# Optimization experiments

Measured on AMD Instinct MI355X. Metric: run time of the kernel, lower is better.

## Reference

```python
import jax, jax.numpy as jnp
import numpy as np

D_MODEL = 1024
EXPAND = 2
D_INNER = EXPAND * D_MODEL   # 2048
D_STATE = 16
D_CONV = 4
DT_RANK = 64                  # ceil(d_model / 16)
BATCH = 2
SEQLEN = 1024
DT_MIN, DT_MAX = 0.001, 0.1


def setup_inputs() -> dict:
    key = jax.random.key(0)
    ks = jax.random.split(key, 10)
    s = 0.02
    # dt bias init per Mamba: inv-softplus of dt sampled log-uniform in [dt_min, dt_max]
    u = jax.random.uniform(ks[0], (D_INNER,), jnp.float32)
    dt = jnp.exp(u * (np.log(DT_MAX) - np.log(DT_MIN)) + np.log(DT_MIN))
    dt = jnp.clip(dt, 1e-4, None)
    inv_dt = dt + jnp.log(-jnp.expm1(-dt))
    dt_std = DT_RANK ** -0.5
    A_log = jnp.log(jnp.tile(jnp.arange(1, D_STATE + 1, dtype=jnp.float32), (D_INNER, 1)))
    return {
        "hidden_states": jax.random.normal(ks[1], (BATCH, SEQLEN, D_MODEL), jnp.float32),
        "in_proj_w": jax.random.normal(ks[2], (2 * D_INNER, D_MODEL), jnp.float32) * s,
        "conv1d_w": jax.random.normal(ks[3], (D_INNER, D_CONV), jnp.float32) * s,
        "conv1d_b": jnp.zeros((D_INNER,), jnp.float32),
        "x_proj_w": jax.random.normal(ks[4], (DT_RANK + 2 * D_STATE, D_INNER), jnp.float32) * s,
        "dt_proj_w": jax.random.uniform(ks[5], (D_INNER, DT_RANK), jnp.float32, -dt_std, dt_std),
        "dt_proj_b": inv_dt,
        "A_log": A_log,
        "D_skip": jnp.ones((D_INNER,), jnp.float32),
        "out_proj_w": jax.random.normal(ks[6], (D_MODEL, D_INNER), jnp.float32) * s,
    }


def _mamba_forward(hidden_states, in_proj_w, conv1d_w, conv1d_b, x_proj_w,
                   dt_proj_w, dt_proj_b, A_log, D_skip, out_proj_w):
    B_, L, _ = hidden_states.shape
    # in_proj: (b, l, d_model) -> (b, l, 2*d_inner); split into x and gate z
    xz = jnp.einsum('bld,ed->ble', hidden_states, in_proj_w)
    x, z = xz[..., :D_INNER], xz[..., D_INNER:]
    # causal depthwise conv1d over time (pad left K-1, truncate to L) + SiLU
    xp = jnp.pad(x, ((0, 0), (D_CONV - 1, 0), (0, 0)))
    xc = conv1d_b
    acc = jnp.zeros_like(x)
    for k in range(D_CONV):  # tiny fixed kernel loop
        acc = acc + conv1d_w[:, k] * xp[:, k:k + L, :]
    xc = jax.nn.silu(acc + conv1d_b)
    # input-dependent dt / B / C
    x_dbl = jnp.einsum('bld,rd->blr', xc, x_proj_w)
    dt_lr = x_dbl[..., :DT_RANK]
    Bm = x_dbl[..., DT_RANK:DT_RANK + D_STATE]        # (b, l, n)
    Cm = x_dbl[..., DT_RANK + D_STATE:]               # (b, l, n)
    delta = jax.nn.softplus(jnp.einsum('blr,dr->bld', dt_lr, dt_proj_w) + dt_proj_b)
    A = -jnp.exp(A_log)                               # (d, n)

    def step(state, inputs):
        delta_t, B_t, C_t, u_t = inputs               # (b,d) (b,n) (b,n) (b,d)
        dA = jnp.exp(delta_t[..., None] * A)          # (b, d, n)
        state = state * dA + (delta_t * u_t)[..., None] * B_t[:, None, :]
        y_t = jnp.einsum('bdn,bn->bd', state, C_t)
        return state, y_t

    init = jnp.zeros((B_, D_INNER, D_STATE), delta.dtype)
    scan_in = (jnp.swapaxes(delta, 0, 1), jnp.swapaxes(Bm, 0, 1),
               jnp.swapaxes(Cm, 0, 1), jnp.swapaxes(xc, 0, 1))
    _, ys = jax.lax.scan(step, init, scan_in)         # ys: (l, b, d)
    y = jnp.swapaxes(ys, 0, 1)
    y = y + xc * D_skip                               # skip connection
    y = y * jax.nn.silu(z)                            # gate
    return jnp.einsum('bld,md->blm', y, out_proj_w)   # out_proj (no bias)


def reference(hidden_states, in_proj_w, conv1d_w, conv1d_b, x_proj_w,
              dt_proj_w, dt_proj_b, A_log, D_skip, out_proj_w):
    return _mamba_forward(hidden_states, in_proj_w, conv1d_w, conv1d_b, x_proj_w,
                          dt_proj_w, dt_proj_b, A_log, D_skip, out_proj_w)
```

## Files before the change

### kernel.cpp

```cpp
#include <hip/hip_runtime.h>
#include <hip/hip_bf16.h>
#include <math.h>
#include <stdint.h>

#define D_MODEL 1024
#define D_INNER 2048
#define D_STATE 16
#define D_CONV  4
#define DT_RANK 64
#define BATCH   2
#define SEQLEN  1024
#define M_TOK   (BATCH * SEQLEN)
#define XDBL_W  (DT_RANK + 2 * D_STATE)
#define CHUNKS  16
#define CLEN    (SEQLEN / CHUNKS)
#define KSPLIT  8

typedef unsigned short us16;
typedef __bf16 bf16x8 __attribute__((ext_vector_type(8)));
typedef float floatx4 __attribute__((ext_vector_type(4)));

__device__ __forceinline__ float silu_f(float v) {
    return v / (1.0f + __expf(-v));
}
__device__ __forceinline__ float softplus_f(float v) {
    return v > 20.0f ? v : log1pf(__expf(v));
}
__device__ __forceinline__ us16 f2bf(float f) {
    unsigned u = __float_as_uint(f);
    u += 0x7FFF + ((u >> 16) & 1);
    return (us16)(u >> 16);
}
__device__ __forceinline__ float bf2f(us16 h) {
    return __uint_as_float(((unsigned)h) << 16);
}

__device__ __forceinline__ void gload_lds16(const us16* g, us16* l) {
    auto* l3 = reinterpret_cast<__attribute__((address_space(3))) us16*>(
        reinterpret_cast<uintptr_t>(l));
    auto* g1 = reinterpret_cast<const __attribute__((address_space(1))) us16*>(
        reinterpret_cast<uintptr_t>(g));
    __builtin_amdgcn_global_load_lds(g1, l3, 16, 0, 0);
}

__global__ __launch_bounds__(256)
void split_bf16(const float* __restrict__ src, us16* __restrict__ hi,
                us16* __restrict__ lo) {
    const int i = (blockIdx.x * 256 + threadIdx.x) * 4;
    const float4 v = *(const float4*)(src + i);
    us16 h0 = f2bf(v.x), h1 = f2bf(v.y), h2 = f2bf(v.z), h3 = f2bf(v.w);
    ushort4 hv = {h0, h1, h2, h3};
    ushort4 lv = {f2bf(v.x - bf2f(h0)), f2bf(v.y - bf2f(h1)),
                  f2bf(v.z - bf2f(h2)), f2bf(v.w - bf2f(h3))};
    *(ushort4*)(hi + i) = hv;
    *(ushort4*)(lo + i) = lv;
}

template<int BN, int MODE>
__global__ __launch_bounds__(256)
void gemm_mfma3(const us16* __restrict__ Ah, const us16* __restrict__ Al,
                const us16* __restrict__ Wh, const us16* __restrict__ Wl,
                int lda, int kLen, float* __restrict__ C0,
                float* __restrict__ C1, int ldc)
{
    constexpr int BM = 128;
    constexpr int NT = BN / 32;
    __shared__ us16 sAh[BM * 32];
    __shared__ us16 sAl[BM * 32];
    __shared__ us16 sWh[BN * 32];
    __shared__ us16 sWl[BN * 32];

    const int tid  = threadIdx.x;
    const int wave = tid >> 6;
    const int lane = tid & 63;
    const int wm   = wave & 1;
    const int wn   = wave >> 1;
    const int m0   = blockIdx.y * BM;
    const int n0   = blockIdx.x * BN;
    const int kBeg = blockIdx.z * kLen;
    const int quad = lane >> 4;
    const int l15  = lane & 15;
    const int sr   = lane >> 2;
    const int spos = lane & 3;

    floatx4 acc[4][NT] = {};

    for (int k0 = 0; k0 < kLen; k0 += 32) {
        __syncthreads();
        {
            int s = wave;
            int row = s * 16 + sr;
            int c = spos ^ ((row >> 1) & 3);
            size_t go = (size_t)(m0 + row) * lda + kBeg + k0 + c * 8;
            gload_lds16(Ah + go, sAh + s * 512);
            gload_lds16(Al + go, sAl + s * 512);
            s = wave + 4;
            row = s * 16 + sr;
            c = spos ^ ((row >> 1) & 3);
            go = (size_t)(m0 + row) * lda + kBeg + k0 + c * 8;
            gload_lds16(Ah + go, sAh + s * 512);
            gload_lds16(Al + go, sAl + s * 512);
        }
        {
            int s = wave;
            int row = s * 16 + sr;
            int c = spos ^ ((row >> 1) & 3);
            size_t go = (size_t)(n0 + row) * lda + kBeg + k0 + c * 8;
            gload_lds16(Wh + go, sWh + s * 512);
            gload_lds16(Wl + go, sWl + s * 512);
            if (BN == 128) {
                s = wave + 4;
                row = s * 16 + sr;
                c = spos ^ ((row >> 1) & 3);
                go = (size_t)(n0 + row) * lda + kBeg + k0 + c * 8;
                gload_lds16(Wh + go, sWh + s * 512);
                gload_lds16(Wl + go, sWl + s * 512);
            }
        }
        __syncthreads();

        bf16x8 ah[4], al[4], bh[NT], bl[NT];
#pragma unroll
        for (int i = 0; i < 4; i++) {
            const int r = wm * 64 + i * 16 + l15;
            const int off = r * 32 + ((quad ^ ((r >> 1) & 3)) * 8);
            ah[i] = *(const bf16x8*)(sAh + off);
            al[i] = *(const bf16x8*)(sAl + off);
        }
#pragma unroll
        for (int j = 0; j < NT; j++) {
            const int r = wn * (BN / 2) + j * 16 + l15;
            const int off = r * 32 + ((quad ^ ((r >> 1) & 3)) * 8);
            bh[j] = *(const bf16x8*)(sWh + off);
            bl[j] = *(const bf16x8*)(sWl + off);
        }
#pragma unroll
        for (int i = 0; i < 4; i++)
#pragma unroll
            for (int j = 0; j < NT; j++) {
                acc[i][j] = __builtin_amdgcn_mfma_f32_16x16x32_bf16(
                    ah[i], bh[j], acc[i][j], 0, 0, 0);
                acc[i][j] = __builtin_amdgcn_mfma_f32_16x16x32_bf16(
                    al[i], bh[j], acc[i][j], 0, 0, 0);
                acc[i][j] = __builtin_amdgcn_mfma_f32_16x16x32_bf16(
                    ah[i], bl[j], acc[i][j], 0, 0, 0);
            }
    }

#pragma unroll
    for (int i = 0; i < 4; i++) {
        const int rowb = m0 + wm * 64 + i * 16 + quad * 4;
#pragma unroll
        for (int j = 0; j < NT; j++) {
            const int col = n0 + wn * (BN / 2) + j * 16 + l15;
#pragma unroll
            for (int r = 0; r < 4; r++) {
                const float v = acc[i][j][r];
                const size_t rr = (size_t)(rowb + r);
                if (MODE == 1) {
                    if (n0 < D_INNER) C0[rr * D_INNER + col] = v;
                    else              C1[rr * D_INNER + (col - D_INNER)] = v;
                } else {
                    C0[((size_t)blockIdx.z * M_TOK + rr) * ldc + col] = v;
                }
            }
        }
    }
}

__global__ __launch_bounds__(256)
void add2_kernel(const float* __restrict__ part, float* __restrict__ out)
{
    const int i = (blockIdx.x * 256 + threadIdx.x) * 4;
    float4 a = *(const float4*)(part + i);
    const float4 b = *(const float4*)(part + (size_t)M_TOK * D_MODEL + i);
    a.x += b.x; a.y += b.y; a.z += b.z; a.w += b.w;
    *(float4*)(out + i) = a;
}

template<int MODE>
__global__ __launch_bounds__(256)
void gemm_nt(const float* __restrict__ A, int lda,
             const float* __restrict__ W, int ldw,
             float* __restrict__ C0, float* __restrict__ C1, int ldc,
             const float* __restrict__ bias,
             int M, int N, int K)
{
    __shared__ float As[16][68];
    __shared__ float Ws[16][68];

    const int tid  = threadIdx.x;
    const int tx   = tid & 15;
    const int ty   = tid >> 4;
    const int n0   = blockIdx.x * 64;
    const int m0   = blockIdx.y * 64;
    const int lrow = tid >> 2;
    const int lkq  = tid & 3;

    float acc[4][4] = {};

    for (int k0 = 0; k0 < K; k0 += 16) {
        const float4 av = *(const float4*)(A + (size_t)(m0 + lrow) * lda + k0 + lkq * 4);
        const int wn = n0 + lrow;
        float4 wv = make_float4(0.f, 0.f, 0.f, 0.f);
        if (wn < N)
            wv = *(const float4*)(W + (size_t)wn * ldw + k0 + lkq * 4);

        __syncthreads();
        As[lkq * 4 + 0][lrow] = av.x;
        As[lkq * 4 + 1][lrow] = av.y;
        As[lkq * 4 + 2][lrow] = av.z;
        As[lkq * 4 + 3][lrow] = av.w;
        Ws[lkq * 4 + 0][lrow] = wv.x;
        Ws[lkq * 4 + 1][lrow] = wv.y;
        Ws[lkq * 4 + 2][lrow] = wv.z;
        Ws[lkq * 4 + 3][lrow] = wv.w;
        __syncthreads();

#pragma unroll
        for (int k = 0; k < 16; k++) {
            const float4 a = *(const float4*)&As[k][ty * 4];
            const float4 w = *(const float4*)&Ws[k][tx * 4];
            const float avv[4] = {a.x, a.y, a.z, a.w};
            const float wvv[4] = {w.x, w.y, w.z, w.w};
#pragma unroll
            for (int i = 0; i < 4; i++)
#pragma unroll
                for (int j = 0; j < 4; j++)
                    acc[i][j] += avv[i] * wvv[j];
        }
    }

    const int mbase = m0 + ty * 4;
    const int nbase = n0 + tx * 4;
#pragma unroll
    for (int i = 0; i < 4; i++) {
#pragma unroll
        for (int j = 0; j < 4; j++) {
            const int n = nbase + j;
            const size_t row = (size_t)(mbase + i);
            if (MODE == 0) {
                if (n < N) C0[row * ldc + n] = acc[i][j];
            } else if (MODE == 2) {
                C0[row * ldc + n] = softplus_f(acc[i][j] + bias[n]);
            }
        }
    }
}

__global__ __launch_bounds__(256)
void gemm_xproj(const float* __restrict__ A, const float* __restrict__ W,
                float* __restrict__ part)
{
    __shared__ float As[16][68];
    __shared__ float Ws[16][68];

    const int tid  = threadIdx.x;
    const int tx   = tid & 15;
    const int ty   = tid >> 4;
    const int n0   = blockIdx.x * 64;
    const int m0   = blockIdx.y * 64;
    const int kz   = blockIdx.z;
    const int lrow = tid >> 2;
    const int lkq  = tid & 3;

    float acc[4][4] = {};
    const int kbeg = kz * (D_INNER / KSPLIT);
    const int kend = kbeg + (D_INNER / KSPLIT);

    for (int k0 = kbeg; k0 < kend; k0 += 16) {
        const float4 av = *(const float4*)(A + (size_t)(m0 + lrow) * D_INNER + k0 + lkq * 4);
        const int wn = n0 + lrow;
        float4 wv = make_float4(0.f, 0.f, 0.f, 0.f);
        if (wn < XDBL_W)
            wv = *(const float4*)(W + (size_t)wn * D_INNER + k0 + lkq * 4);

        __syncthreads();
        As[lkq * 4 + 0][lrow] = av.x;
        As[lkq * 4 + 1][lrow] = av.y;
        As[lkq * 4 + 2][lrow] = av.z;
        As[lkq * 4 + 3][lrow] = av.w;
        Ws[lkq * 4 + 0][lrow] = wv.x;
        Ws[lkq * 4 + 1][lrow] = wv.y;
        Ws[lkq * 4 + 2][lrow] = wv.z;
        Ws[lkq * 4 + 3][lrow] = wv.w;
        __syncthreads();

#pragma unroll
        for (int k = 0; k < 16; k++) {
            const float4 a = *(const float4*)&As[k][ty * 4];
            const float4 w = *(const float4*)&Ws[k][tx * 4];
            const float avv[4] = {a.x, a.y, a.z, a.w};
            const float wvv[4] = {w.x, w.y, w.z, w.w};
#pragma unroll
            for (int i = 0; i < 4; i++)
#pragma unroll
                for (int j = 0; j < 4; j++)
                    acc[i][j] += avv[i] * wvv[j];
        }
    }

    const int mbase = m0 + ty * 4;
    const int nbase = n0 + tx * 4;
#pragma unroll
    for (int i = 0; i < 4; i++)
#pragma unroll
        for (int j = 0; j < 4; j++) {
            const int n = nbase + j;
            if (n < XDBL_W)
                part[((size_t)kz * M_TOK + mbase + i) * XDBL_W + n] = acc[i][j];
        }
}

__global__ __launch_bounds__(256)
void xproj_reduce(const float* __restrict__ part, float* __restrict__ xdbl)
{
    const int i = blockIdx.x * 256 + threadIdx.x;
    float s = 0.f;
#pragma unroll
    for (int k = 0; k < KSPLIT; k++)
        s += part[(size_t)k * M_TOK * XDBL_W + i];
    xdbl[i] = s;
}

__global__ __launch_bounds__(256)
void conv_silu_kernel(const float* __restrict__ x, const float* __restrict__ w,
                      const float* __restrict__ bias, float* __restrict__ xc)
{
    const int idx = blockIdx.x * 256 + threadIdx.x;
    const int d = idx & (D_INNER - 1);
    const int t = (idx >> 11) & (SEQLEN - 1);
    const int b = idx >> 21;
    float acc = bias[d];
#pragma unroll
    for (int k = 0; k < D_CONV; k++) {
        const int tt = t - (D_CONV - 1) + k;
        if (tt >= 0)
            acc += w[d * D_CONV + k] * x[((size_t)b * SEQLEN + tt) * D_INNER + d];
    }
    xc[idx] = silu_f(acc);
}

__global__ __launch_bounds__(256)
void scan_part(const float* __restrict__ delta, const float* __restrict__ xdbl,
               const float* __restrict__ xc, const float* __restrict__ A_log,
               float* __restrict__ P, float* __restrict__ S)
{
    const int g = blockIdx.x * 256 + threadIdx.x;
    const int d = g & (D_INNER - 1);
    const int c = (g >> 11) & (CHUNKS - 1);
    const int b = g >> 15;

    float An[D_STATE];
#pragma unroll
    for (int n = 0; n < D_STATE; n++)
        An[n] = -__expf(A_log[d * D_STATE + n]);

    float p[D_STATE], s[D_STATE];
#pragma unroll
    for (int n = 0; n < D_STATE; n++) { p[n] = 1.f; s[n] = 0.f; }

    const size_t row0 = (size_t)b * SEQLEN + c * CLEN;
    for (int t = 0; t < CLEN; t++) {
        const size_t row = row0 + t;
        const float dlt  = delta[row * D_INNER + d];
        const float dltu = dlt * xc[row * D_INNER + d];
        const float4* Bp = (const float4*)(xdbl + row * XDBL_W + DT_RANK);
        const float4 B0 = Bp[0], B1 = Bp[1], B2 = Bp[2], B3 = Bp[3];
        const float Bv[D_STATE] = {B0.x, B0.y, B0.z, B0.w, B1.x, B1.y, B1.z, B1.w,
                                   B2.x, B2.y, B2.z, B2.w, B3.x, B3.y, B3.z, B3.w};
#pragma unroll
        for (int n = 0; n < D_STATE; n++) {
            const float a = __expf(dlt * An[n]);
            s[n] = s[n] * a + dltu * Bv[n];
            p[n] *= a;
        }
    }

    const size_t base = ((size_t)(b * CHUNKS + c) * D_STATE) * D_INNER + d;
#pragma unroll
    for (int n = 0; n < D_STATE; n++) {
        P[base + (size_t)n * D_INNER] = p[n];
        S[base + (size_t)n * D_INNER] = s[n];
    }
}

__global__ __launch_bounds__(256)
void scan_apply(const float* __restrict__ delta, const float* __restrict__ xdbl,
                const float* __restrict__ xc, const float* __restrict__ A_log,
                const float* __restrict__ D_skip,
                const float* __restrict__ P, const float* __restrict__ S,
                const float* __restrict__ z,
                us16* __restrict__ yh, us16* __restrict__ yl)
{
    const int g = blockIdx.x * 256 + threadIdx.x;
    const int d = g & (D_INNER - 1);
    const int c = (g >> 11) & (CHUNKS - 1);
    const int b = g >> 15;

    float An[D_STATE];
#pragma unroll
    for (int n = 0; n < D_STATE; n++)
        An[n] = -__expf(A_log[d * D_STATE + n]);

    float st[D_STATE];
#pragma unroll
    for (int n = 0; n < D_STATE; n++) st[n] = 0.f;
    for (int j = 0; j < c; j++) {
        const size_t base = ((size_t)(b * CHUNKS + j) * D_STATE) * D_INNER + d;
#pragma unroll
        for (int n = 0; n < D_STATE; n++) {
            const size_t idx = base + (size_t)n * D_INNER;
            st[n] = S[idx] + P[idx] * st[n];
        }
    }

    const float Dv = D_skip[d];
    const size_t row0 = (size_t)b * SEQLEN + c * CLEN;
    for (int t = 0; t < CLEN; t++) {
        const size_t row = row0 + t;
        const float dlt  = delta[row * D_INNER + d];
        const float u    = xc[row * D_INNER + d];
        const float dltu = dlt * u;
        const float4* Bp = (const float4*)(xdbl + row * XDBL_W + DT_RANK);
        const float4 B0 = Bp[0], B1 = Bp[1], B2 = Bp[2], B3 = Bp[3];
        const float4* Cp = (const float4*)(xdbl + row * XDBL_W + DT_RANK + D_STATE);
        const float4 C0 = Cp[0], C1 = Cp[1], C2 = Cp[2], C3 = Cp[3];
        const float Bv[D_STATE] = {B0.x, B0.y, B0.z, B0.w, B1.x, B1.y, B1.z, B1.w,
                                   B2.x, B2.y, B2.z, B2.w, B3.x, B3.y, B3.z, B3.w};
        const float Cv[D_STATE] = {C0.x, C0.y, C0.z, C0.w, C1.x, C1.y, C1.z, C1.w,
                                   C2.x, C2.y, C2.z, C2.w, C3.x, C3.y, C3.z, C3.w};
        float y = 0.f;
#pragma unroll
        for (int n = 0; n < D_STATE; n++) {
            const float a = __expf(dlt * An[n]);
            st[n] = st[n] * a + dltu * Bv[n];
            y += st[n] * Cv[n];
        }
        const float yv = (y + u * Dv) * silu_f(z[row * D_INNER + d]);
        const us16 h = f2bf(yv);
        yh[row * D_INNER + d] = h;
        yl[row * D_INNER + d] = f2bf(yv - bf2f(h));
    }
}

extern "C" void kernel_launch(void* const* d_in, const int* in_sizes, int n_in,
                              void* d_out, int out_size, void* d_ws, size_t ws_size,
                              hipStream_t stream)
{
    const float* hs         = (const float*)d_in[0];
    const float* in_proj_w  = (const float*)d_in[1];
    const float* conv_w     = (const float*)d_in[2];
    const float* conv_b     = (const float*)d_in[3];
    const float* x_proj_w   = (const float*)d_in[4];
    const float* dt_proj_w  = (const float*)d_in[5];
    const float* dt_proj_b  = (const float*)d_in[6];
    const float* A_log      = (const float*)d_in[7];
    const float* D_skip     = (const float*)d_in[8];
    const float* out_proj_w = (const float*)d_in[9];
    float* out = (float*)d_out;

    char* base = (char*)d_ws;
    const size_t MB = 1u << 20;
    float* xbuf  = (float*)(base);
    float* zbuf  = (float*)(base + 16 * MB);
    float* xcbuf = (float*)(base + 32 * MB);
    float* opart = (float*)(base + 32 * MB);
    float* xdbl  = (float*)(base + 48 * MB);
    float* Pbuf  = (float*)(base + 49 * MB);
    float* Sbuf  = (float*)(base + 53 * MB);
    us16*  hsh   = (us16*)(base + 57 * MB);
    us16*  hsl   = (us16*)(base + 61 * MB);
    float* part  = (float*)(base + 57 * MB);
    us16*  iwh   = (us16*)(base + 65 * MB);
    us16*  iwl   = (us16*)(base + 73 * MB);
    us16*  ybh   = (us16*)(base + 65 * MB);
    us16*  ybl   = (us16*)(base + 73 * MB);
    us16*  owh   = (us16*)(base + 81 * MB);
    us16*  owl   = (us16*)(base + 85 * MB);

    const dim3 blk(256);

    split_bf16<<<(M_TOK * D_MODEL) / 1024, blk, 0, stream>>>(hs, hsh, hsl);
    split_bf16<<<(2 * D_INNER * D_MODEL) / 1024, blk, 0, stream>>>(in_proj_w, iwh, iwl);
    split_bf16<<<(D_MODEL * D_INNER) / 1024, blk, 0, stream>>>(out_proj_w, owh, owl);

    gemm_mfma3<128, 1><<<dim3((2 * D_INNER) / 128, M_TOK / 128), blk, 0, stream>>>(
        hsh, hsl, iwh, iwl, D_MODEL, D_MODEL, xbuf, zbuf, D_INNER);

    conv_silu_kernel<<<(BATCH * SEQLEN * D_INNER) / 256, blk, 0, stream>>>(
        xbuf, conv_w, conv_b, xcbuf);

    gemm_xproj<<<dim3(2, M_TOK / 64, KSPLIT), blk, 0, stream>>>(
        xcbuf, x_proj_w, part);
    xproj_reduce<<<(M_TOK * XDBL_W) / 256, blk, 0, stream>>>(part, xdbl);

    gemm_nt<2><<<dim3(D_INNER / 64, M_TOK / 64), blk, 0, stream>>>(
        xdbl, XDBL_W, dt_proj_w, DT_RANK, xbuf, nullptr, D_INNER, dt_proj_b,
        M_TOK, D_INNER, DT_RANK);

    scan_part<<<(BATCH * CHUNKS * D_INNER) / 256, blk, 0, stream>>>(
        xbuf, xdbl, xcbuf, A_log, Pbuf, Sbuf);
    scan_apply<<<(BATCH * CHUNKS * D_INNER) / 256, blk, 0, stream>>>(
        xbuf, xdbl, xcbuf, A_log, D_skip, Pbuf, Sbuf, zbuf, ybh, ybl);

    gemm_mfma3<64, 2><<<dim3(D_MODEL / 64, M_TOK / 128, 2), blk, 0, stream>>>(
        ybh, ybl, owh, owl, D_INNER, D_INNER / 2, opart, nullptr, D_MODEL);
    add2_kernel<<<(M_TOK * D_MODEL) / 1024, blk, 0, stream>>>(opart, out);
}
```

Before: 369.4 us.

## Split scan into 64 chunks with a separate chunk-prefix kernel

Raises the chunk count of the selective scan from 16 to 64, so four times as many threads each walk a shorter segment. A new scan_prefix kernel computes the carried-in state for every chunk once and writes it over P, replacing the per-thread loop in scan_apply that re-combined all preceding chunks. The workspace layout is reshuffled to make room for the larger P/S buffers, the out_proj weight split is moved later so its buffer is not overwritten, and the time loops gain unroll pragmas. This costs an extra launch and more P/S traffic, and relies on the buffer aliasing staying correct.

```diff
diff --git a/kernel.cpp b/kernel.cpp
--- a/kernel.cpp
+++ b/kernel.cpp
@@ -12,7 +12,7 @@
 #define SEQLEN  1024
 #define M_TOK   (BATCH * SEQLEN)
 #define XDBL_W  (DT_RANK + 2 * D_STATE)
-#define CHUNKS  16
+#define CHUNKS  64
 #define CLEN    (SEQLEN / CHUNKS)
 #define KSPLIT  8
 
@@ -349,7 +349,7 @@
     const int g = blockIdx.x * 256 + threadIdx.x;
     const int d = g & (D_INNER - 1);
     const int c = (g >> 11) & (CHUNKS - 1);
-    const int b = g >> 15;
+    const int b = g >> 17;
 
     float An[D_STATE];
 #pragma unroll
@@ -361,6 +361,7 @@
     for (int n = 0; n < D_STATE; n++) { p[n] = 1.f; s[n] = 0.f; }
 
     const size_t row0 = (size_t)b * SEQLEN + c * CLEN;
+#pragma unroll 4
     for (int t = 0; t < CLEN; t++) {
         const size_t row = row0 + t;
         const float dlt  = delta[row * D_INNER + d];
@@ -386,17 +387,35 @@
 }
 
 __global__ __launch_bounds__(256)
+void scan_prefix(float* PH, const float* __restrict__ S)
+{
+    const int g = blockIdx.x * 256 + threadIdx.x;
+    const int d = g & (D_INNER - 1);
+    const int n = (g >> 11) & (D_STATE - 1);
+    const int b = g >> 15;
+
+    float h = 0.f;
+    for (int c = 0; c < CHUNKS; c++) {
+        const size_t idx = ((size_t)(b * CHUNKS + c) * D_STATE + n) * D_INNER + d;
+        const float p = PH[idx];
+        const float s = S[idx];
+        PH[idx] = h;
+        h = s + p * h;
+    }
+}
+
+__global__ __launch_bounds__(256)
 void scan_apply(const float* __restrict__ delta, const float* __restrict__ xdbl,
                 const float* __restrict__ xc, const float* __restrict__ A_log,
                 const float* __restrict__ D_skip,
-                const float* __restrict__ P, const float* __restrict__ S,
+                const float* __restrict__ H,
                 const float* __restrict__ z,
                 us16* __restrict__ yh, us16* __restrict__ yl)
 {
     const int g = blockIdx.x * 256 + threadIdx.x;
     const int d = g & (D_INNER - 1);
     const int c = (g >> 11) & (CHUNKS - 1);
-    const int b = g >> 15;
+    const int b = g >> 17;
 
     float An[D_STATE];
 #pragma unroll
@@ -404,19 +423,14 @@
         An[n] = -__expf(A_log[d * D_STATE + n]);
 
     float st[D_STATE];
-#pragma unroll
-    for (int n = 0; n < D_STATE; n++) st[n] = 0.f;
-    for (int j = 0; j < c; j++) {
-        const size_t base = ((size_t)(b * CHUNKS + j) * D_STATE) * D_INNER + d;
-#pragma unroll
-        for (int n = 0; n < D_STATE; n++) {
-            const size_t idx = base + (size_t)n * D_INNER;
-            st[n] = S[idx] + P[idx] * st[n];
-        }
-    }
+    const size_t hbase = ((size_t)(b * CHUNKS + c) * D_STATE) * D_INNER + d;
+#pragma unroll
+    for (int n = 0; n < D_STATE; n++)
+        st[n] = H[hbase + (size_t)n * D_INNER];
 
     const float Dv = D_skip[d];
     const size_t row0 = (size_t)b * SEQLEN + c * CLEN;
+#pragma unroll 4
     for (int t = 0; t < CLEN; t++) {
         const size_t row = row0 + t;
         const float dlt  = delta[row * D_INNER + d];
@@ -467,15 +481,15 @@
     float* xcbuf = (float*)(base + 32 * MB);
     float* opart = (float*)(base + 32 * MB);
     float* xdbl  = (float*)(base + 48 * MB);
+    us16*  iwh   = (us16*)(base + 49 * MB);
+    us16*  iwl   = (us16*)(base + 57 * MB);
     float* Pbuf  = (float*)(base + 49 * MB);
-    float* Sbuf  = (float*)(base + 53 * MB);
-    us16*  hsh   = (us16*)(base + 57 * MB);
-    us16*  hsl   = (us16*)(base + 61 * MB);
-    float* part  = (float*)(base + 57 * MB);
-    us16*  iwh   = (us16*)(base + 65 * MB);
-    us16*  iwl   = (us16*)(base + 73 * MB);
+    float* Sbuf  = (float*)(base + 65 * MB);
     us16*  ybh   = (us16*)(base + 65 * MB);
     us16*  ybl   = (us16*)(base + 73 * MB);
+    us16*  hsh   = (us16*)(base + 81 * MB);
+    us16*  hsl   = (us16*)(base + 85 * MB);
+    float* part  = (float*)(base + 81 * MB);
     us16*  owh   = (us16*)(base + 81 * MB);
     us16*  owl   = (us16*)(base + 85 * MB);
 
@@ -483,7 +497,6 @@
 
     split_bf16<<<(M_TOK * D_MODEL) / 1024, blk, 0, stream>>>(hs, hsh, hsl);
     split_bf16<<<(2 * D_INNER * D_MODEL) / 1024, blk, 0, stream>>>(in_proj_w, iwh, iwl);
-    split_bf16<<<(D_MODEL * D_INNER) / 1024, blk, 0, stream>>>(out_proj_w, owh, owl);
 
     gemm_mfma3<128, 1><<<dim3((2 * D_INNER) / 128, M_TOK / 128), blk, 0, stream>>>(
         hsh, hsl, iwh, iwl, D_MODEL, D_MODEL, xbuf, zbuf, D_INNER);
@@ -495,14 +508,18 @@
         xcbuf, x_proj_w, part);
     xproj_reduce<<<(M_TOK * XDBL_W) / 256, blk, 0, stream>>>(part, xdbl);
 
+    split_bf16<<<(D_MODEL * D_INNER) / 1024, blk, 0, stream>>>(out_proj_w, owh, owl);
+
     gemm_nt<2><<<dim3(D_INNER / 64, M_TOK / 64), blk, 0, stream>>>(
         xdbl, XDBL_W, dt_proj_w, DT_RANK, xbuf, nullptr, D_INNER, dt_proj_b,
         M_TOK, D_INNER, DT_RANK);
 
     scan_part<<<(BATCH * CHUNKS * D_INNER) / 256, blk, 0, stream>>>(
         xbuf, xdbl, xcbuf, A_log, Pbuf, Sbuf);
+    scan_prefix<<<(BATCH * D_STATE * D_INNER) / 256, blk, 0, stream>>>(
+        Pbuf, Sbuf);
     scan_apply<<<(BATCH * CHUNKS * D_INNER) / 256, blk, 0, stream>>>(
-        xbuf, xdbl, xcbuf, A_log, D_skip, Pbuf, Sbuf, zbuf, ybh, ybl);
+        xbuf, xdbl, xcbuf, A_log, D_skip, Pbuf, zbuf, ybh, ybl);
 
     gemm_mfma3<64, 2><<<dim3(D_MODEL / 64, M_TOK / 128, 2), blk, 0, stream>>>(
         ybh, ybl, owh, owl, D_INNER, D_INNER / 2, opart, nullptr, D_MODEL);
```

After: 336.9 us. 1.1x faster.
